# Performance work log

Measured on AMD Instinct MI355X. Metric: run time of the kernel, lower is better.

The kernel has to match this reference:

```python
import jax, jax.numpy as jnp
import numpy as np

TAU = 0.07
EMA = 0.99


def _l2norm(x, eps=1e-12):
    n = jnp.linalg.norm(x, axis=-1, keepdims=True)
    return x / jnp.maximum(n, eps)


def setup_inputs() -> dict:
    key = jax.random.key(0)
    k1, k2, k3, k4, k5 = jax.random.split(key, 5)
    B, Cs, Ct, H, W, d, M = 32, 256, 512, 64, 64, 128, 16
    fs4 = jax.random.normal(k1, (B, Cs, H, W), jnp.float32)
    ft = jax.random.normal(k2, (B, Ct, H // 2, W // 2), jnp.float32)
    Ws = jax.random.normal(k3, (d, Cs), jnp.float32) * 0.02  # 1x1 conv weight
    Wt = jax.random.normal(k4, (d, Ct), jnp.float32) * 0.02
    C = _l2norm(jax.random.normal(k5, (M, d), jnp.float32))  # unit-norm codebook
    return {"fs4": fs4, "ft": ft, "Ws": Ws, "Wt": Wt, "C": C}


def reference(fs4, ft, Ws, Wt, C):
    B, _, H, W = fs4.shape
    d = Ws.shape[0]
    M = C.shape[0]
    # bilinear upsample teacher features to student resolution (align_corners=False)
    ft_up = jax.image.resize(ft, (B, ft.shape[1], H, W), method="bilinear")
    # 1x1 convs == per-pixel GEMMs; flatten spatial -> [B, HW, d]
    s = jnp.einsum("bchw,dc->bhwd", fs4, Ws).reshape(B, H * W, d)
    t = jnp.einsum("bchw,dc->bhwd", ft_up, Wt).reshape(B, H * W, d)
    zs = _l2norm(s)
    zt = jax.lax.stop_gradient(_l2norm(t))  # teacher path is no_grad
    Cng = jax.lax.stop_gradient(C)  # codebook is a buffer (no grad)
    # soft prototype assignment
    qt = jax.nn.softmax(jnp.einsum("bnd,md->bnm", zt, Cng) / TAU, axis=-1)
    ht = qt.mean(axis=1)  # [B, M]
    # EMA codebook update (no grad)
    qt_f = qt.reshape(-1, M)
    zt_f = zt.reshape(-1, d)
    denom = qt_f.sum(axis=0) + 1e-6  # [M]
    mu = _l2norm(jnp.einsum("nm,nd->md", qt_f, zt_f) / denom[:, None])
    C_new = _l2norm(EMA * Cng + (1.0 - EMA) * mu)
    # student assignment (grad flows through zs)
    qs = jax.nn.softmax(jnp.einsum("bnd,md->bnm", zs, Cng) / TAU, axis=-1)
    hs = qs.mean(axis=1)  # [B, M]
    # F.kl_div(log(hs+1e-12), ht, reduction='batchmean') = sum(ht*(log ht - log hs))/B
    kl = (jax.scipy.special.xlogy(ht, ht) - ht * jnp.log(hs + 1e-12)).sum() / B
    return kl, jax.lax.stop_gradient(C_new)
```

## Files before the change

### kernel.cpp

```cpp
#include <hip/hip_runtime.h>
#include <math.h>

#define TAU_INV 14.285714285714286f

using short8 = __attribute__((ext_vector_type(8))) short;
using f32x4  = __attribute__((ext_vector_type(4))) float;

#define WS_HS   0
#define WS_HT   512
#define WS_MU   1024
#define WS_TL   4096
#define WS_TLC  (4096 + 32*1024*128)
#define WS_WSH  (WS_TLC + 32*1024*16)
#define WS_WSL  (WS_WSH + 20480)
#define WS_WTH  (WS_WSL + 20480)
#define WS_WTL  (WS_WTH + 40960)

__device__ __forceinline__ uint bf16rne(float f) {
    uint u = __float_as_uint(f);
    return (u + 0x7fffu + ((u >> 16) & 1u)) >> 16;
}

__global__ __launch_bounds__(256) void prep_kernel(
    const float* __restrict__ C, const float* __restrict__ Ws, const float* __restrict__ Wt,
    ushort* __restrict__ Wsh, ushort* __restrict__ Wsl,
    ushort* __restrict__ Wth, ushort* __restrict__ Wtl)
{
    int id = blockIdx.x * 256 + threadIdx.x;
    float v; ushort* H; ushort* L; int idx;
    if (id < 160*256) {
        int row = id >> 8, c = id & 255;
        if (row < 128) v = Ws[row*256 + c];
        else if (row < 144) {
            v = 0.f; int m = row - 128;
            #pragma unroll 8
            for (int dd = 0; dd < 128; dd++) v = fmaf(C[m*128+dd], Ws[dd*256 + c], v);
        } else v = 0.f;
        H = Wsh; L = Wsl; idx = id;
    } else {
        int id2 = id - 160*256;
        int row = id2 >> 9, c = id2 & 511;
        if (row < 128) v = Wt[row*512 + c];
        else if (row < 144) {
            v = 0.f; int m = row - 128;
            #pragma unroll 8
            for (int dd = 0; dd < 128; dd++) v = fmaf(C[m*128+dd], Wt[dd*512 + c], v);
        } else v = 0.f;
        H = Wth; L = Wtl; idx = id2;
    }
    uint h = bf16rne(v);
    float hf = __uint_as_float(h << 16);
    uint l = bf16rne(v - hf);
    H[idx] = (ushort)h; L[idx] = (ushort)l;
}

template<bool STUDENT, int CIN, int HW>
__global__ __launch_bounds__(256, 2) void gemm_kernel(
    const float* __restrict__ X, const ushort* __restrict__ Wh, const ushort* __restrict__ Wl,
    float* __restrict__ hs_acc, float* __restrict__ tl, float* __restrict__ tlC)
{
    __shared__ __align__(16) ushort Ah[144*32];
    __shared__ __align__(16) ushort Al[144*32];
    __shared__ __align__(16) uint   Bpk[128*32];
    __shared__ float nrm2_lds[128];

    const int tid  = threadIdx.x;
    const int lane = tid & 63;
    const int w    = tid >> 6, wd = w >> 1, wn = w & 1;
    const int g    = lane >> 4, m16 = lane & 15;
    const int ST   = (wd == 0) ? 5 : 4;
    const int tiles_b = HW / 128;
    const int b   = blockIdx.x / tiles_b;
    const int n0  = (blockIdx.x % tiles_b) * 128;
    const float* Xb = X + (size_t)b * CIN * HW + n0;

    f32x4 acc[5][4];
    #pragma unroll
    for (int i = 0; i < 5; i++)
        #pragma unroll
        for (int j = 0; j < 4; j++) acc[i][j] = (f32x4){0.f, 0.f, 0.f, 0.f};

    const int cb = (tid & 7) * 4;
    const int nf = tid >> 3;

    for (int k0 = 0; k0 < CIN; k0 += 32) {
        #pragma unroll
        for (int r = 0; r < 3; r++) {
            int id = tid + r * 256;
            if (r < 2 || id < 576) {
                int row = id >> 2, slot = id & 3;
                int dst = row * 32 + ((slot ^ (row & 3)) << 3);
                int src = row * CIN + k0 + slot * 8;
                *(uint4*)&Ah[dst] = *(const uint4*)&Wh[src];
                *(uint4*)&Al[dst] = *(const uint4*)&Wl[src];
            }
        }
        float4 vv[4];
        #pragma unroll
        for (int i = 0; i < 4; i++)
            vv[i] = *(const float4*)&Xb[(size_t)(k0 + cb + i) * HW + nf * 4];
        #pragma unroll
        for (int j = 0; j < 4; j++) {
            uint q[4];
            #pragma unroll
            for (int i = 0; i < 4; i++) {
                float f = (j == 0) ? vv[i].x : (j == 1) ? vv[i].y : (j == 2) ? vv[i].z : vv[i].w;
                uint h = bf16rne(f);
                float hf = __uint_as_float(h << 16);
                uint lo = bf16rne(f - hf);
                q[i] = (h << 16) | lo;
            }
            int row = nf * 4 + j;
            int dst = row * 32 + (((tid & 7) ^ (nf & 7)) << 2);
            *(uint4*)&Bpk[dst] = make_uint4(q[0], q[1], q[2], q[3]);
        }
        __syncthreads();

        short8 ah[5], al[5];
        #pragma unroll
        for (int ti = 0; ti < 5; ti++) {
            if (ti < ST) {
                int row = wd * 80 + ti * 16 + m16;
                int ad = row * 32 + ((g ^ (row & 3)) << 3);
                ah[ti] = *(const short8*)&Ah[ad];
                al[ti] = *(const short8*)&Al[ad];
            }
        }
        #pragma unroll
        for (int nj = 0; nj < 4; nj++) {
            int row = wn * 64 + nj * 16 + m16;
            int key = (row >> 2) & 7;
            const uint4 q0 = *(const uint4*)&Bpk[row * 32 + (((2*g)   ^ key) << 2)];
            const uint4 q1 = *(const uint4*)&Bpk[row * 32 + (((2*g+1) ^ key) << 2)];
            uint4 bhv, blv;
            bhv.x = __builtin_amdgcn_perm(q0.y, q0.x, 0x07060302u);
            bhv.y = __builtin_amdgcn_perm(q0.w, q0.z, 0x07060302u);
            bhv.z = __builtin_amdgcn_perm(q1.y, q1.x, 0x07060302u);
            bhv.w = __builtin_amdgcn_perm(q1.w, q1.z, 0x07060302u);
            blv.x = __builtin_amdgcn_perm(q0.y, q0.x, 0x05040100u);
            blv.y = __builtin_amdgcn_perm(q0.w, q0.z, 0x05040100u);
            blv.z = __builtin_amdgcn_perm(q1.y, q1.x, 0x05040100u);
            blv.w = __builtin_amdgcn_perm(q1.w, q1.z, 0x05040100u);
            short8 bh = *(short8*)&bhv;
            short8 bl = *(short8*)&blv;
            #pragma unroll
            for (int ti = 0; ti < 5; ti++) {
                if (ti < ST) {
                    acc[ti][nj] = __builtin_amdgcn_mfma_f32_16x16x32_bf16(ah[ti], bh, acc[ti][nj], 0, 0, 0);
                    acc[ti][nj] = __builtin_amdgcn_mfma_f32_16x16x32_bf16(al[ti], bh, acc[ti][nj], 0, 0, 0);
                    acc[ti][nj] = __builtin_amdgcn_mfma_f32_16x16x32_bf16(ah[ti], bl, acc[ti][nj], 0, 0, 0);
                }
            }
        }
        __syncthreads();
    }

    if constexpr (STUDENT) {
        float nrm_own[4];
        #pragma unroll
        for (int nj = 0; nj < 4; nj++) {
            float v = 0.f;
            int st = (wd == 0) ? 5 : 3;
            #pragma unroll
            for (int ti = 0; ti < 5; ti++) {
                if (ti < st) {
                    f32x4 a = acc[ti][nj];
                    v = fmaf(a.x, a.x, v); v = fmaf(a.y, a.y, v);
                    v = fmaf(a.z, a.z, v); v = fmaf(a.w, a.w, v);
                }
            }
            v += __shfl_xor(v, 16); v += __shfl_xor(v, 32);
            nrm_own[nj] = v;
        }
        if (wd == 0 && g == 0) {
            #pragma unroll
            for (int nj = 0; nj < 4; nj++)
                nrm2_lds[wn * 64 + nj * 16 + m16] = nrm_own[nj];
        }
        __syncthreads();
        if (wd == 1) {
            float hsl[4] = {0.f, 0.f, 0.f, 0.f};
            #pragma unroll
            for (int nj = 0; nj < 4; nj++) {
                int nloc = wn * 64 + nj * 16 + m16;
                float nrm2 = nrm2_lds[nloc] + nrm_own[nj];
                float sc = TAU_INV / fmaxf(sqrtf(nrm2), 1e-12f);
                float e0 = acc[3][nj].x * sc, e1 = acc[3][nj].y * sc;
                float e2 = acc[3][nj].z * sc, e3 = acc[3][nj].w * sc;
                float mx = fmaxf(fmaxf(e0, e1), fmaxf(e2, e3));
                mx = fmaxf(mx, __shfl_xor(mx, 16)); mx = fmaxf(mx, __shfl_xor(mx, 32));
                e0 = expf(e0 - mx); e1 = expf(e1 - mx); e2 = expf(e2 - mx); e3 = expf(e3 - mx);
                float s = e0 + e1 + e2 + e3;
                s += __shfl_xor(s, 16); s += __shfl_xor(s, 32);
                float is = 1.f / s;
                hsl[0] = fmaf(e0, is, hsl[0]); hsl[1] = fmaf(e1, is, hsl[1]);
                hsl[2] = fmaf(e2, is, hsl[2]); hsl[3] = fmaf(e3, is, hsl[3]);
            }
            #pragma unroll
            for (int r = 0; r < 4; r++) {
                float v = hsl[r];
                v += __shfl_xor(v, 1); v += __shfl_xor(v, 2);
                v += __shfl_xor(v, 4); v += __shfl_xor(v, 8);
                if (m16 == 0) atomicAdd(&hs_acc[b * 16 + 4 * g + r], v);
            }
        }
    } else {
        #pragma unroll
        for (int ti = 0; ti < 5; ti++) {
            if (ti < ST) {
                int d0 = wd * 80 + ti * 16;
                #pragma unroll
                for (int nj = 0; nj < 4; nj++) {
                    int n = n0 + wn * 64 + nj * 16 + m16;
                    if (d0 < 128)
                        *(f32x4*)&tl[((size_t)(b * 1024 + n)) * 128 + d0 + 4 * g] = acc[ti][nj];
                    else
                        *(f32x4*)&tlC[((size_t)(b * 1024 + n)) * 16 + 4 * g] = acc[ti][nj];
                }
            }
        }
    }
}

__global__ __launch_bounds__(256) void teacher_highres_kernel(
    const float* __restrict__ tl, const float* __restrict__ tlC,
    float* __restrict__ ht_acc, float* __restrict__ mu_acc)
{
    __shared__ float t_s[64][132];
    __shared__ float qs_s[64][16];
    __shared__ float inv_s[64];
    int tid = threadIdx.x;
    int b = blockIdx.x >> 4, y0 = (blockIdx.x & 15) * 4;

    int p = tid >> 2, q = tid & 3;
    int jx = p >> 1;
    int c0, c1; float wx0, wx1;
    if ((p & 1) == 0) { c0 = jx - 1; c1 = jx;     wx0 = 0.25f; wx1 = 0.75f; }
    else              { c0 = jx;     c1 = jx + 1; wx0 = 0.75f; wx1 = 0.25f; }
    c0 = max(c0, 0); c1 = min(c1, 31);

    int mm = tid >> 4, d8 = (tid & 15) * 8;
    float a8[8] = {0.f,0.f,0.f,0.f,0.f,0.f,0.f,0.f};
    float htl = 0.f;
    size_t base = (size_t)b * 1024;

    for (int ry = 0; ry < 4; ry++) {
        int y = y0 + ry;
        int jy = y >> 1;
        int r0, r1; float wy0, wy1;
        if ((y & 1) == 0) { r0 = jy - 1; r1 = jy;     wy0 = 0.25f; wy1 = 0.75f; }
        else              { r0 = jy;     r1 = jy + 1; wy0 = 0.75f; wy1 = 0.25f; }
        r0 = max(r0, 0); r1 = min(r1, 31);

        const float* v00 = tl + (base + r0*32 + c0)*128 + q*32;
        const float* v01 = tl + (base + r0*32 + c1)*128 + q*32;
        const float* v10 = tl + (base + r1*32 + c0)*128 + q*32;
        const float* v11 = tl + (base + r1*32 + c1)*128 + q*32;

        float tc[32];
        float nr = 0.f;
        #pragma unroll
        for (int i = 0; i < 32; i += 4) {
            float4 a  = *(const float4*)(v00+i);
            float4 bb = *(const float4*)(v01+i);
            float4 cc = *(const float4*)(v10+i);
            float4 dd = *(const float4*)(v11+i);
            float t0 = wy0*fmaf(wx0,a.x,wx1*bb.x) + wy1*fmaf(wx0,cc.x,wx1*dd.x);
            float t1 = wy0*fmaf(wx0,a.y,wx1*bb.y) + wy1*fmaf(wx0,cc.y,wx1*dd.y);
            float t2 = wy0*fmaf(wx0,a.z,wx1*bb.z) + wy1*fmaf(wx0,cc.z,wx1*dd.z);
            float t3 = wy0*fmaf(wx0,a.w,wx1*bb.w) + wy1*fmaf(wx0,cc.w,wx1*dd.w);
            tc[i]=t0; tc[i+1]=t1; tc[i+2]=t2; tc[i+3]=t3;
            nr += t0*t0 + t1*t1 + t2*t2 + t3*t3;
        }
        nr += __shfl_xor(nr, 1);
        nr += __shfl_xor(nr, 2);
        float inv = 1.f / fmaxf(sqrtf(nr), 1e-12f);
        #pragma unroll
        for (int i = 0; i < 32; i += 4) {
            float4 o = {tc[i], tc[i+1], tc[i+2], tc[i+3]};
            *(float4*)&t_s[p][q*32+i] = o;
        }
        if (q == 0) inv_s[p] = inv;
        __syncthreads();

        if (q == 0) {
            const float* g00 = tlC + (base + r0*32 + c0)*16;
            const float* g01 = tlC + (base + r0*32 + c1)*16;
            const float* g10 = tlC + (base + r1*32 + c0)*16;
            const float* g11 = tlC + (base + r1*32 + c1)*16;
            float e[16]; float mx = -1e30f;
            #pragma unroll
            for (int m = 0; m < 16; m++) {
                float l = wy0*fmaf(wx0,g00[m],wx1*g01[m]) + wy1*fmaf(wx0,g10[m],wx1*g11[m]);
                e[m] = l * inv * TAU_INV;
                mx = fmaxf(mx, e[m]);
            }
            float sum = 0.f;
            #pragma unroll
            for (int m = 0; m < 16; m++) { e[m] = expf(e[m] - mx); sum += e[m]; }
            float isum = 1.f / sum;
            #pragma unroll
            for (int m = 0; m < 16; m++) qs_s[p][m] = e[m] * isum;
        }
        __syncthreads();

        for (int pp = 0; pp < 64; pp++) {
            float qraw = qs_s[pp][mm];
            if ((tid & 15) == 0) htl += qraw;
            float qv = qraw * inv_s[pp];
            float4 t0 = *(const float4*)&t_s[pp][d8];
            float4 t1 = *(const float4*)&t_s[pp][d8+4];
            a8[0] = fmaf(qv, t0.x, a8[0]); a8[1] = fmaf(qv, t0.y, a8[1]);
            a8[2] = fmaf(qv, t0.z, a8[2]); a8[3] = fmaf(qv, t0.w, a8[3]);
            a8[4] = fmaf(qv, t1.x, a8[4]); a8[5] = fmaf(qv, t1.y, a8[5]);
            a8[6] = fmaf(qv, t1.z, a8[6]); a8[7] = fmaf(qv, t1.w, a8[7]);
        }
        __syncthreads();
    }
    #pragma unroll
    for (int j = 0; j < 8; j++) atomicAdd(&mu_acc[mm*128 + d8 + j], a8[j]);
    if ((tid & 15) == 0) atomicAdd(&ht_acc[b*16 + mm], htl);
}

__global__ __launch_bounds__(256) void finalize_kernel(
    const float* __restrict__ C, const float* __restrict__ hs_acc,
    const float* __restrict__ ht_acc, const float* __restrict__ mu_acc,
    float* __restrict__ out)
{
    __shared__ float denom_s[16];
    __shared__ float red[256];
    int tid = threadIdx.x;
    if (tid < 16) {
        float s = 0.f;
        #pragma unroll
        for (int bb = 0; bb < 32; bb++) s += ht_acc[bb*16 + tid];
        denom_s[tid] = s + 1e-6f;
    }
    __syncthreads();
    int m = tid >> 4, dbase = (tid & 15) * 8;
    float v[8]; float ss = 0.f;
    #pragma unroll
    for (int j = 0; j < 8; j++) {
        v[j] = mu_acc[m*128 + dbase + j] / denom_s[m];
        ss = fmaf(v[j], v[j], ss);
    }
    ss += __shfl_xor(ss, 1); ss += __shfl_xor(ss, 2);
    ss += __shfl_xor(ss, 4); ss += __shfl_xor(ss, 8);
    float invn = 1.f / fmaxf(sqrtf(ss), 1e-12f);
    float cn[8]; float cs = 0.f;
    #pragma unroll
    for (int j = 0; j < 8; j++) {
        cn[j] = 0.99f * C[m*128 + dbase + j] + 0.01f * (v[j] * invn);
        cs = fmaf(cn[j], cn[j], cs);
    }
    cs += __shfl_xor(cs, 1); cs += __shfl_xor(cs, 2);
    cs += __shfl_xor(cs, 4); cs += __shfl_xor(cs, 8);
    float invc = 1.f / fmaxf(sqrtf(cs), 1e-12f);
    #pragma unroll
    for (int j = 0; j < 8; j++) out[1 + m*128 + dbase + j] = cn[j] * invc;

    float kacc = 0.f;
    for (int idx = tid; idx < 512; idx += 256) {
        float htv = ht_acc[idx] * (1.f/4096.f);
        float hsv = hs_acc[idx] * (1.f/4096.f);
        float t1 = (htv > 0.f) ? htv * logf(htv) : 0.f;
        kacc += t1 - htv * logf(hsv + 1e-12f);
    }
    red[tid] = kacc;
    __syncthreads();
    for (int s2 = 128; s2 > 0; s2 >>= 1) {
        if (tid < s2) red[tid] += red[tid + s2];
        __syncthreads();
    }
    if (tid == 0) out[0] = red[0] * (1.f/32.f);
}

extern "C" void kernel_launch(void* const* d_in, const int* in_sizes, int n_in,
                              void* d_out, int out_size, void* d_ws, size_t ws_size,
                              hipStream_t stream) {
    const float* fs4 = (const float*)d_in[0];
    const float* ft  = (const float*)d_in[1];
    const float* Ws  = (const float*)d_in[2];
    const float* Wt  = (const float*)d_in[3];
    const float* C   = (const float*)d_in[4];
    float* out = (float*)d_out;
    float* ws  = (float*)d_ws;
    float* hs_acc = ws + WS_HS;
    float* ht_acc = ws + WS_HT;
    float* mu_acc = ws + WS_MU;
    float* tl  = ws + WS_TL;
    float* tlC = ws + WS_TLC;
    ushort* Wsh = (ushort*)(ws + WS_WSH);
    ushort* Wsl = (ushort*)(ws + WS_WSL);
    ushort* Wth = (ushort*)(ws + WS_WTH);
    ushort* Wtl = (ushort*)(ws + WS_WTL);

    hipMemsetAsync(ws, 0, 3072 * sizeof(float), stream);
    hipLaunchKernelGGL(prep_kernel, dim3(480), dim3(256), 0, stream,
                       C, Ws, Wt, Wsh, Wsl, Wth, Wtl);
    hipLaunchKernelGGL((gemm_kernel<true, 256, 4096>), dim3(1024), dim3(256), 0, stream,
                       fs4, Wsh, Wsl, hs_acc, nullptr, nullptr);
    hipLaunchKernelGGL((gemm_kernel<false, 512, 1024>), dim3(256), dim3(256), 0, stream,
                       ft, Wth, Wtl, nullptr, tl, tlC);
    hipLaunchKernelGGL(teacher_highres_kernel, dim3(512), dim3(256), 0, stream,
                       tl, tlC, ht_acc, mu_acc);
    hipLaunchKernelGGL(finalize_kernel, dim3(1), dim3(256), 0, stream,
                       C, hs_acc, ht_acc, mu_acc, out);
}
```

Baseline: 462.5 us.

## Restructure teacher high-res kernel to wave-per-row with sliding bilinear window

The teacher upsample kernel is rewritten so that each wavefront handles half an output row. Each lane owns two channels, and the horizontal bilinear neighbours are reused through a sliding register window. Softmax and norm reductions move to wave shuffles, removing the shared-memory tiles and the block barriers inside the pixel loop. The mu accumulation goes through shared-memory atomics and then into 8 global slices that finalize sums, to cut global atomic contention. In exchange there are many more shuffle operations per pixel, and shared and global float atomics make the summation order nondeterministic.

```diff
diff --git a/kernel.cpp b/kernel.cpp
--- a/kernel.cpp
+++ b/kernel.cpp
@@ -8,9 +8,9 @@
 
 #define WS_HS   0
 #define WS_HT   512
-#define WS_MU   1024
-#define WS_TL   4096
-#define WS_TLC  (4096 + 32*1024*128)
+#define WS_MUS  1024
+#define WS_TL   17408
+#define WS_TLC  (17408 + 32*1024*128)
 #define WS_WSH  (WS_TLC + 32*1024*16)
 #define WS_WSL  (WS_WSH + 20480)
 #define WS_WTH  (WS_WSL + 20480)
@@ -224,107 +224,110 @@
 
 __global__ __launch_bounds__(256) void teacher_highres_kernel(
     const float* __restrict__ tl, const float* __restrict__ tlC,
-    float* __restrict__ ht_acc, float* __restrict__ mu_acc)
+    float* __restrict__ ht_acc, float* __restrict__ mus)
 {
-    __shared__ float t_s[64][132];
-    __shared__ float qs_s[64][16];
-    __shared__ float inv_s[64];
+    __shared__ float muL[2048];
     int tid = threadIdx.x;
-    int b = blockIdx.x >> 4, y0 = (blockIdx.x & 15) * 4;
-
-    int p = tid >> 2, q = tid & 3;
-    int jx = p >> 1;
-    int c0, c1; float wx0, wx1;
-    if ((p & 1) == 0) { c0 = jx - 1; c1 = jx;     wx0 = 0.25f; wx1 = 0.75f; }
-    else              { c0 = jx;     c1 = jx + 1; wx0 = 0.75f; wx1 = 0.25f; }
-    c0 = max(c0, 0); c1 = min(c1, 31);
-
-    int mm = tid >> 4, d8 = (tid & 15) * 8;
-    float a8[8] = {0.f,0.f,0.f,0.f,0.f,0.f,0.f,0.f};
+    int b  = blockIdx.x >> 5;
+    int bg = blockIdx.x & 31;
+    int w  = tid >> 6, lane = tid & 63;
+    int W  = bg * 4 + w;
+    int y  = W >> 1;
+    int x0 = (W & 1) * 32;
+
+    #pragma unroll
+    for (int i = 0; i < 8; i++) muL[tid + i*256] = 0.f;
+    __syncthreads();
+
+    int jy = y >> 1; int r0, r1; float wy0, wy1;
+    if ((y & 1) == 0) { r0 = max(jy-1, 0); r1 = jy;            wy0 = 0.25f; wy1 = 0.75f; }
+    else              { r0 = jy;           r1 = min(jy+1, 31); wy0 = 0.75f; wy1 = 0.25f; }
+
+    size_t rb0 = (size_t)b*1024 + r0*32;
+    size_t rb1 = (size_t)b*1024 + r1*32;
+    int d0 = lane * 2;
+    int ml = lane & 15;
+
+    float acc[16][2];
+    #pragma unroll
+    for (int m = 0; m < 16; m++) { acc[m][0] = 0.f; acc[m][1] = 0.f; }
     float htl = 0.f;
-    size_t base = (size_t)b * 1024;
-
-    for (int ry = 0; ry < 4; ry++) {
-        int y = y0 + ry;
-        int jy = y >> 1;
-        int r0, r1; float wy0, wy1;
-        if ((y & 1) == 0) { r0 = jy - 1; r1 = jy;     wy0 = 0.25f; wy1 = 0.75f; }
-        else              { r0 = jy;     r1 = jy + 1; wy0 = 0.75f; wy1 = 0.25f; }
-        r0 = max(r0, 0); r1 = min(r1, 31);
-
-        const float* v00 = tl + (base + r0*32 + c0)*128 + q*32;
-        const float* v01 = tl + (base + r0*32 + c1)*128 + q*32;
-        const float* v10 = tl + (base + r1*32 + c0)*128 + q*32;
-        const float* v11 = tl + (base + r1*32 + c1)*128 + q*32;
-
-        float tc[32];
-        float nr = 0.f;
-        #pragma unroll
-        for (int i = 0; i < 32; i += 4) {
-            float4 a  = *(const float4*)(v00+i);
-            float4 bb = *(const float4*)(v01+i);
-            float4 cc = *(const float4*)(v10+i);
-            float4 dd = *(const float4*)(v11+i);
-            float t0 = wy0*fmaf(wx0,a.x,wx1*bb.x) + wy1*fmaf(wx0,cc.x,wx1*dd.x);
-            float t1 = wy0*fmaf(wx0,a.y,wx1*bb.y) + wy1*fmaf(wx0,cc.y,wx1*dd.y);
-            float t2 = wy0*fmaf(wx0,a.z,wx1*bb.z) + wy1*fmaf(wx0,cc.z,wx1*dd.z);
-            float t3 = wy0*fmaf(wx0,a.w,wx1*bb.w) + wy1*fmaf(wx0,cc.w,wx1*dd.w);
-            tc[i]=t0; tc[i+1]=t1; tc[i+2]=t2; tc[i+3]=t3;
-            nr += t0*t0 + t1*t1 + t2*t2 + t3*t3;
-        }
-        nr += __shfl_xor(nr, 1);
-        nr += __shfl_xor(nr, 2);
+
+    float cva0, cva1, cla, cvb0, cvb1, clb;
+    {
+        int c = max((x0 >> 1) - 1, 0);
+        float2 u0 = *(const float2*)&tl[(rb0 + c)*128 + d0];
+        float2 u1 = *(const float2*)&tl[(rb1 + c)*128 + d0];
+        cva0 = wy0*u0.x + wy1*u1.x; cva1 = wy0*u0.y + wy1*u1.y;
+        cla  = wy0*tlC[(rb0 + c)*16 + ml] + wy1*tlC[(rb1 + c)*16 + ml];
+    }
+    {
+        int c = x0 >> 1;
+        float2 u0 = *(const float2*)&tl[(rb0 + c)*128 + d0];
+        float2 u1 = *(const float2*)&tl[(rb1 + c)*128 + d0];
+        cvb0 = wy0*u0.x + wy1*u1.x; cvb1 = wy0*u0.y + wy1*u1.y;
+        clb  = wy0*tlC[(rb0 + c)*16 + ml] + wy1*tlC[(rb1 + c)*16 + ml];
+    }
+
+    for (int xi = 0; xi < 32; xi++) {
+        int x = x0 + xi;
+        float t0, t1, lg;
+        if ((x & 1) == 0) {
+            t0 = 0.25f*cva0 + 0.75f*cvb0;
+            t1 = 0.25f*cva1 + 0.75f*cvb1;
+            lg = 0.25f*cla  + 0.75f*clb;
+        } else {
+            int c = min((x >> 1) + 1, 31);
+            float2 u0 = *(const float2*)&tl[(rb0 + c)*128 + d0];
+            float2 u1 = *(const float2*)&tl[(rb1 + c)*128 + d0];
+            float cvc0 = wy0*u0.x + wy1*u1.x;
+            float cvc1 = wy0*u0.y + wy1*u1.y;
+            float clc  = wy0*tlC[(rb0 + c)*16 + ml] + wy1*tlC[(rb1 + c)*16 + ml];
+            t0 = 0.75f*cvb0 + 0.25f*cvc0;
+            t1 = 0.75f*cvb1 + 0.25f*cvc1;
+            lg = 0.75f*clb  + 0.25f*clc;
+            cva0 = cvb0; cva1 = cvb1; cla = clb;
+            cvb0 = cvc0; cvb1 = cvc1; clb = clc;
+        }
+        float nr = t0*t0 + t1*t1;
+        nr += __shfl_xor(nr, 1);  nr += __shfl_xor(nr, 2);  nr += __shfl_xor(nr, 4);
+        nr += __shfl_xor(nr, 8);  nr += __shfl_xor(nr, 16); nr += __shfl_xor(nr, 32);
         float inv = 1.f / fmaxf(sqrtf(nr), 1e-12f);
-        #pragma unroll
-        for (int i = 0; i < 32; i += 4) {
-            float4 o = {tc[i], tc[i+1], tc[i+2], tc[i+3]};
-            *(float4*)&t_s[p][q*32+i] = o;
-        }
-        if (q == 0) inv_s[p] = inv;
-        __syncthreads();
-
-        if (q == 0) {
-            const float* g00 = tlC + (base + r0*32 + c0)*16;
-            const float* g01 = tlC + (base + r0*32 + c1)*16;
-            const float* g10 = tlC + (base + r1*32 + c0)*16;
-            const float* g11 = tlC + (base + r1*32 + c1)*16;
-            float e[16]; float mx = -1e30f;
-            #pragma unroll
-            for (int m = 0; m < 16; m++) {
-                float l = wy0*fmaf(wx0,g00[m],wx1*g01[m]) + wy1*fmaf(wx0,g10[m],wx1*g11[m]);
-                e[m] = l * inv * TAU_INV;
-                mx = fmaxf(mx, e[m]);
-            }
-            float sum = 0.f;
-            #pragma unroll
-            for (int m = 0; m < 16; m++) { e[m] = expf(e[m] - mx); sum += e[m]; }
-            float isum = 1.f / sum;
-            #pragma unroll
-            for (int m = 0; m < 16; m++) qs_s[p][m] = e[m] * isum;
-        }
-        __syncthreads();
-
-        for (int pp = 0; pp < 64; pp++) {
-            float qraw = qs_s[pp][mm];
-            if ((tid & 15) == 0) htl += qraw;
-            float qv = qraw * inv_s[pp];
-            float4 t0 = *(const float4*)&t_s[pp][d8];
-            float4 t1 = *(const float4*)&t_s[pp][d8+4];
-            a8[0] = fmaf(qv, t0.x, a8[0]); a8[1] = fmaf(qv, t0.y, a8[1]);
-            a8[2] = fmaf(qv, t0.z, a8[2]); a8[3] = fmaf(qv, t0.w, a8[3]);
-            a8[4] = fmaf(qv, t1.x, a8[4]); a8[5] = fmaf(qv, t1.y, a8[5]);
-            a8[6] = fmaf(qv, t1.z, a8[6]); a8[7] = fmaf(qv, t1.w, a8[7]);
-        }
-        __syncthreads();
-    }
-    #pragma unroll
-    for (int j = 0; j < 8; j++) atomicAdd(&mu_acc[mm*128 + d8 + j], a8[j]);
-    if ((tid & 15) == 0) atomicAdd(&ht_acc[b*16 + mm], htl);
+        float e = lg * inv * TAU_INV;
+        float mx = e;
+        mx = fmaxf(mx, __shfl_xor(mx, 1)); mx = fmaxf(mx, __shfl_xor(mx, 2));
+        mx = fmaxf(mx, __shfl_xor(mx, 4)); mx = fmaxf(mx, __shfl_xor(mx, 8));
+        float ee = expf(e - mx);
+        float s = ee;
+        s += __shfl_xor(s, 1); s += __shfl_xor(s, 2); s += __shfl_xor(s, 4); s += __shfl_xor(s, 8);
+        float qt = ee / s;
+        htl += qt;
+        float qs = qt * inv;
+        #pragma unroll
+        for (int m = 0; m < 16; m++) {
+            float qv = __shfl(qs, m);
+            acc[m][0] = fmaf(qv, t0, acc[m][0]);
+            acc[m][1] = fmaf(qv, t1, acc[m][1]);
+        }
+    }
+    #pragma unroll
+    for (int m = 0; m < 16; m++) {
+        atomicAdd(&muL[m*128 + d0],     acc[m][0]);
+        atomicAdd(&muL[m*128 + d0 + 1], acc[m][1]);
+    }
+    if (lane < 16) atomicAdd(&ht_acc[b*16 + ml], htl);
+    __syncthreads();
+    float* slice = mus + (b & 7) * 2048;
+    #pragma unroll
+    for (int i = 0; i < 8; i++) {
+        int idx = tid + i*256;
+        atomicAdd(&slice[idx], muL[idx]);
+    }
 }
 
 __global__ __launch_bounds__(256) void finalize_kernel(
     const float* __restrict__ C, const float* __restrict__ hs_acc,
-    const float* __restrict__ ht_acc, const float* __restrict__ mu_acc,
+    const float* __restrict__ ht_acc, const float* __restrict__ mus,
     float* __restrict__ out)
 {
     __shared__ float denom_s[16];
@@ -338,10 +341,19 @@
     }
     __syncthreads();
     int m = tid >> 4, dbase = (tid & 15) * 8;
-    float v[8]; float ss = 0.f;
+    float v[8] = {0.f,0.f,0.f,0.f,0.f,0.f,0.f,0.f};
+    #pragma unroll
+    for (int sl = 0; sl < 8; sl++) {
+        const float* p = mus + sl*2048 + m*128 + dbase;
+        float4 a = *(const float4*)p;
+        float4 bq = *(const float4*)(p + 4);
+        v[0] += a.x;  v[1] += a.y;  v[2] += a.z;  v[3] += a.w;
+        v[4] += bq.x; v[5] += bq.y; v[6] += bq.z; v[7] += bq.w;
+    }
+    float ss = 0.f;
     #pragma unroll
     for (int j = 0; j < 8; j++) {
-        v[j] = mu_acc[m*128 + dbase + j] / denom_s[m];
+        v[j] = v[j] / denom_s[m];
         ss = fmaf(v[j], v[j], ss);
     }
     ss += __shfl_xor(ss, 1); ss += __shfl_xor(ss, 2);
@@ -387,7 +399,7 @@
     float* ws  = (float*)d_ws;
     float* hs_acc = ws + WS_HS;
     float* ht_acc = ws + WS_HT;
-    float* mu_acc = ws + WS_MU;
+    float* mus = ws + WS_MUS;
     float* tl  = ws + WS_TL;
     float* tlC = ws + WS_TLC;
     ushort* Wsh = (ushort*)(ws + WS_WSH);
@@ -395,15 +407,15 @@
     ushort* Wth = (ushort*)(ws + WS_WTH);
     ushort* Wtl = (ushort*)(ws + WS_WTL);
 
-    hipMemsetAsync(ws, 0, 3072 * sizeof(float), stream);
+    hipMemsetAsync(ws, 0, 17408 * sizeof(float), stream);
     hipLaunchKernelGGL(prep_kernel, dim3(480), dim3(256), 0, stream,
                        C, Ws, Wt, Wsh, Wsl, Wth, Wtl);
     hipLaunchKernelGGL((gemm_kernel<true, 256, 4096>), dim3(1024), dim3(256), 0, stream,
                        fs4, Wsh, Wsl, hs_acc, nullptr, nullptr);
     hipLaunchKernelGGL((gemm_kernel<false, 512, 1024>), dim3(256), dim3(256), 0, stream,
                        ft, Wth, Wtl, nullptr, tl, tlC);
-    hipLaunchKernelGGL(teacher_highres_kernel, dim3(512), dim3(256), 0, stream,
-                       tl, tlC, ht_acc, mu_acc);
+    hipLaunchKernelGGL(teacher_highres_kernel, dim3(1024), dim3(256), 0, stream,
+                       tl, tlC, ht_acc, mus);
     hipLaunchKernelGGL(finalize_kernel, dim3(1), dim3(256), 0, stream,
-                       C, hs_acc, ht_acc, mu_acc, out);
-}
+                       C, hs_acc, ht_acc, mus, out);
+}
```

Result: faster. 419.3 us (-9.3%).
